# Performance work log

Hardware: AMD Instinct MI355X
Metric: run time of the kernel (lower is better)

The kernel has to match this reference:

```python
import jax, jax.numpy as jnp
import numpy as np

SIGMA = 0.002  # TreeEnergyLoss default; edge weight = exp(-||df||^2 / sigma)


def bilinear_resize(x, oh, ow):
    """F.interpolate(mode='bilinear', align_corners=False), no antialias. x: [B,C,H,W]."""
    B, C, H, W = x.shape
    if (H, W) == (oh, ow):
        return x
    def coords(o, n):
        s = (jnp.arange(o, dtype=jnp.float32) + 0.5) * (n / o) - 0.5
        s = jnp.clip(s, 0.0, n - 1.0)
        lo = jnp.floor(s).astype(jnp.int32)
        hi = jnp.minimum(lo + 1, n - 1)
        return lo, hi, s - lo.astype(jnp.float32)
    r0, r1, rf = coords(oh, H)
    c0, c1, cf = coords(ow, W)
    xr = x[:, :, r0, :] * (1.0 - rf)[None, None, :, None] + x[:, :, r1, :] * rf[None, None, :, None]
    return xr[:, :, :, c0] * (1.0 - cf) + xr[:, :, :, c1] * cf


def nearest_resize(x, oh, ow):
    B, C, H, W = x.shape
    if (H, W) == (oh, ow):
        return x
    ri = jnp.floor(jnp.arange(oh) * (H / oh)).astype(jnp.int32)
    ci = jnp.floor(jnp.arange(ow) * (W / ow)).astype(jnp.int32)
    return x[:, :, ri, :][:, :, :, ci]


def _mst_bfs_np(embed, H, W):
    """Kruskal MST on the 4-connected pixel grid (edge cost = squared L2 feature
    distance, as in MinimumSpanningTree(TreeFilter2D.norm2_distance)), then BFS
    order from vertex 0. embed: np [C,H,W]. Returns (sorted_index, sorted_parent)
    where sorted_parent is the BFS position of each vertex's parent."""
    V = H * W
    idx = np.arange(V).reshape(H, W)
    eu = np.concatenate([idx[:-1, :].ravel(), idx[:, :-1].ravel()])
    ev = np.concatenate([idx[1:, :].ravel(), idx[:, 1:].ravel()])
    f = embed.reshape(embed.shape[0], V)
    cost = ((f[:, eu] - f[:, ev]) ** 2).sum(0)
    parent = np.arange(V)
    def find(x):
        root = x
        while parent[root] != root:
            root = parent[root]
        while parent[x] != root:
            parent[x], x = root, parent[x]
        return root
    nbr = [[] for _ in range(V)]
    cnt = 0
    for e in np.argsort(cost, kind='stable'):
        u, v = int(eu[e]), int(ev[e])
        ru, rv = find(u), find(v)
        if ru != rv:
            parent[ru] = rv
            nbr[u].append(v)
            nbr[v].append(u)
            cnt += 1
            if cnt == V - 1:
                break
    sorted_index = np.empty(V, np.int32)
    sorted_parent = np.empty(V, np.int32)
    visited = np.zeros(V, bool)
    sorted_index[0] = 0; sorted_parent[0] = 0; visited[0] = True
    head, tail = 0, 1
    while head < tail:
        u = int(sorted_index[head])
        for v in nbr[u]:
            if not visited[v]:
                visited[v] = True
                sorted_index[tail] = v
                sorted_parent[tail] = head
                tail += 1
        head += 1
    return sorted_index, sorted_parent


def build_trees(embed):
    """embed: [B,C,H,W]. Host-side MST+BFS per batch element (torch.no_grad in original)."""
    e = np.asarray(jax.lax.stop_gradient(embed), dtype=np.float64)
    B, C, H, W = e.shape
    si, sp = zip(*[_mst_bfs_np(e[b], H, W) for b in range(B)])
    return jnp.asarray(np.stack(si)), jnp.asarray(np.stack(sp))


def _tree_filter_single(f, embed, sorted_index, sorted_parent):
    """Normalized tree filter: out_i = sum_j W_ij f_j / sum_j W_ij with
    W_ij = prod of exp(-||de||^2/sigma) along the unique tree path i->j.
    Computed exactly via bottom-up aggregation + top-down propagation in BFS order.
    f: [C,V], embed: [Ce,V]."""
    C, V = f.shape
    fs = f[:, sorted_index]                        # [C,V] features in BFS order
    es = embed[:, sorted_index]
    d = ((es - es[:, sorted_parent]) ** 2).sum(0)  # [V]; d[0]=0 (root self edge)
    w = jnp.exp(-d / SIGMA)                        # edge weight to parent
    # bottom-up: children have larger BFS index, so reverse order is valid.
    # extra ones-row carries the normalizer Z through the same recursion.
    S0 = jnp.concatenate([fs, jnp.ones((1, V), fs.dtype)], axis=0)
    def up(S, j):
        return S.at[:, sorted_parent[j]].add(w[j] * S[:, j]), None
    S, _ = jax.lax.scan(up, S0, jnp.arange(V - 1, 0, -1))
    # top-down: A_root = S_root; A_j = S_j + w_j * (A_parent - w_j * S_j)
    def down(A, j):
        p = sorted_parent[j]
        return A.at[:, j].set(S[:, j] + w[j] * (A[:, p] - w[j] * S[:, j])), None
    A0 = jnp.zeros_like(S).at[:, 0].set(S[:, 0])
    A, _ = jax.lax.scan(down, A0, jnp.arange(1, V))
    out_sorted = A[:C] / A[C]
    return jnp.zeros_like(f).at[:, sorted_index].set(out_sorted)


def tree_filter(feature, embed, si, sp):
    B, C, h, w = feature.shape
    out = jax.vmap(_tree_filter_single)(
        feature.reshape(B, C, h * w),
        embed.reshape(B, embed.shape[1], h * w), si, sp)
    return out.reshape(B, C, h, w)


def setup_inputs():
    key = jax.random.key(0)
    k1, k2, k3, k4 = jax.random.split(key, 4)
    preds = jax.random.normal(k1, (8, 21, 80, 80), jnp.float32)
    # scaled so exp(-||df||^2 / 0.002) gives non-degenerate edge weights
    low_feats = jax.random.uniform(k2, (8, 3, 80, 80), jnp.float32) * 0.02
    high_feats = jax.random.normal(k3, (8, 256, 80, 80), jnp.float32) * 0.002
    unlabeled_ROIs = jax.random.randint(k4, (8, 80, 80), 0, 2, dtype=jnp.int32)
    return {"preds": preds, "low_feats": low_feats,
            "high_feats": high_feats, "unlabeled_ROIs": unlabeled_ROIs}


def reference(preds, low_feats, high_feats, unlabeled_ROIs):
    B, C, h, w = preds.shape
    low = bilinear_resize(low_feats, h, w)  # under torch.no_grad in original
    roi = nearest_resize(unlabeled_ROIs[:, None].astype(jnp.float32), h, w)
    si_l, sp_l = build_trees(low)
    si_h, sp_h = build_trees(high_feats)
    prob = jax.nn.softmax(preds, axis=1)
    AS = tree_filter(prob, jax.lax.stop_gradient(low), si_l, sp_l)  # low-level tree
    AS = tree_filter(AS, high_feats, si_h, sp_h)                    # high-level tree
    N = roi.sum()
    loss = (roi * jnp.abs(prob - AS)).sum()
    return jnp.where(N > 0, loss / N, jnp.zeros((), preds.dtype))  # weight = 1.0
```

## Files before the change

### kernel.cpp

```cpp
#include <hip/hip_runtime.h>

#define BB 8
#define CP 21
#define CF 22
#define CLOW 3
#define CHIGH 256
#define WW 80
#define VV 6400
#define EVERT 6320
#define EE 12640
#define TT 16
#define SIGMA_F 0.002f
#define ROOT 3240

#define NE (VV - 1)
#define NA (2 * NE)
#define NILA 0xFFFFu
#define NB 200

__device__ __forceinline__ void edge_uv(int e, int& u, int& v) {
  if (e < EVERT) { u = e; v = e + WW; }
  else { int e2 = e - EVERT; int r = e2 / (WW - 1); int c = e2 - r * (WW - 1); u = r * WW + c; v = u + 1; }
}

__global__ void k_edgekey(const float* __restrict__ low, const float* __restrict__ high,
                          unsigned long long* __restrict__ ekey) {
  int i = blockIdx.x * blockDim.x + threadIdx.x;
  if (i >= TT * EE) return;
  int t = i / EE, e = i - t * EE;
  int u, v; edge_uv(e, u, v);
  double acc = 0.0;
  if (t < BB) {
    const float* emb = low + (size_t)t * CLOW * VV;
    for (int c = 0; c < CLOW; c++) { double d = (double)emb[c * VV + u] - (double)emb[c * VV + v]; acc += d * d; }
  } else {
    const float* emb = high + (size_t)(t - BB) * CHIGH * VV;
    for (int c = 0; c < CHIGH; c++) { double d = (double)emb[c * VV + u] - (double)emb[c * VV + v]; acc += d * d; }
  }
  unsigned long long bits = (unsigned long long)__double_as_longlong(acc);
  ekey[i] = (bits & ~0x3FFFULL) | (unsigned long long)e;
}

__global__ __launch_bounds__(1024) void k_msttree(const unsigned long long* __restrict__ ekey,
    int* __restrict__ mstU, int* __restrict__ mstV,
    int* __restrict__ ordG, int* __restrict__ spG,
    int* __restrict__ lpG, int* __restrict__ nlevG, float* __restrict__ wvp,
    const float* __restrict__ preds, float* __restrict__ prob) {
  if (blockIdx.x >= TT) {
    int i = (blockIdx.x - TT) * 1024 + threadIdx.x;
    if (i < BB * VV) {
      int b = i / VV, v = i - b * VV;
      const float* p = preds + (size_t)b * CP * VV + v;
      float m = -1e30f;
      #pragma unroll
      for (int c = 0; c < CP; c++) m = fmaxf(m, p[c * VV]);
      float e[CP], s = 0.f;
      #pragma unroll
      for (int c = 0; c < CP; c++) { float x = expf(p[c * VV] - m); e[c] = x; s += x; }
      float inv = 1.f / s;
      float* o = prob + (size_t)b * CP * VV + v;
      #pragma unroll
      for (int c = 0; c < CP; c++) o[c * VV] = e[c] * inv;
    }
    return;
  }
  int t = blockIdx.x;
  const unsigned long long* key = ekey + (size_t)t * EE;
  int* mu = mstU + t * VV;
  int* mv = mstV + t * VV;
  int tid = threadIdx.x;
  const int nt = 1024;
  int lane = tid & 63, wid = tid >> 6;

  __shared__ alignas(16) char arena[152960];
  __shared__ int lasts, spackU, spackW, scenter, smaxd, changed, cnt, necnt, nrcnt;

  int* comp = (int*)(arena + 0);
  unsigned long long* bst = (unsigned long long*)(arena + 25600);
  unsigned short* el0 = (unsigned short*)(arena + 76800);
  unsigned short* el1 = (unsigned short*)(arena + 102080);
  unsigned short* rl0 = (unsigned short*)(arena + 127360);
  unsigned short* rl1 = (unsigned short*)(arena + 140160);

  char* buf = arena;
  int* deg = (int*)(buf + 0);
  int* off = (int*)(buf + 25600);
  unsigned short* adjA = (unsigned short*)(buf + 51208);
  unsigned short* succ = (unsigned short*)(buf + 102408);
  int* pk0 = (int*)(buf + 0);
  int* pk1 = (int*)(buf + 51208);
  unsigned short* r_a = (unsigned short*)(buf + 102408);
  short* H = (short*)(buf + 51208);
  unsigned short* depthR = (unsigned short*)(buf + 76808);
  unsigned short* firstK = (unsigned short*)(buf + 89608);
  short* prefmin = (short*)(buf + 0);
  short* sufmin  = (short*)(buf + 25600);
  unsigned short* distU = (unsigned short*)(buf + 76808);
  unsigned short* parentS = (unsigned short*)(buf + 76808);
  int* lev = (int*)(buf + 0);
  int* cur = (int*)(buf + 25604);
  unsigned short* ordS = (unsigned short*)(buf + 51208);
  unsigned short* posS = (unsigned short*)(buf + 64008);
  int* part = (int*)(buf + 128016);
  short* tbl = (short*)(buf + 128272);
  unsigned short* dbuf2 = (unsigned short*)(buf + 131472);

  auto blockScanEx = [&](int s) -> int {
    int x = s;
    #pragma unroll
    for (int d = 1; d < 64; d <<= 1) { int o = __shfl_up(x, d); if (lane >= d) x += o; }
    if (lane == 63) part[wid] = x;
    __syncthreads();
    if (wid == 0) {
      int y = (lane < 16) ? part[lane] : 0;
      #pragma unroll
      for (int d = 1; d < 16; d <<= 1) { int o = __shfl_up(y, d); if (lane >= d) y += o; }
      if (lane < 16) part[lane] = y;
    }
    __syncthreads();
    int base = (wid > 0) ? part[wid - 1] : 0;
    return base + (x - s);
  };

  for (int v = tid; v < VV; v += nt) { comp[v] = v; bst[v] = ~0ULL; }
  for (int e = tid; e < EE; e += nt) el0[e] = (unsigned short)e;
  for (int v = tid; v < VV; v += nt) rl0[v] = (unsigned short)v;
  if (tid == 0) cnt = 0;
  __syncthreads();
  {
    unsigned short *els = el0, *eld = el1;
    unsigned short *rls = rl0, *rld = rl1;
    int ecnt = EE, rcnt = VV;
    for (int round = 0; round < 48 && ecnt > 0; round++) {
      if (tid == 0) { changed = 0; necnt = 0; nrcnt = 0; }
      for (int j = tid; j < ecnt; j += nt) {
        int e = els[j];
        int u, v; edge_uv(e, u, v);
        int ru = comp[u], rv = comp[v];
        if (ru != rv) { unsigned long long k = key[e]; atomicMin(&bst[ru], k); atomicMin(&bst[rv], k); }
      }
      __syncthreads();
      unsigned short* tgtJ = eld;
      for (int j = tid; j < rcnt; j += nt) {
        int c = rls[j];
        unsigned short tg = (unsigned short)NILA;
        unsigned long long k = bst[c];
        if (k != ~0ULL) {
          int e = (int)(k & 0x3FFFULL);
          int u, v; edge_uv(e, u, v);
          int cu = comp[u], cv = comp[v];
          tg = (unsigned short)((cu == c) ? cv : cu);
        }
        tgtJ[j] = tg;
      }
      __syncthreads();
      for (int j = tid; j < rcnt; j += nt) {
        int c = rls[j];
        int o = tgtJ[j];
        if (o == (int)NILA) continue;
        unsigned long long k = bst[c];
        if (bst[o] == k && c < o) continue;
        comp[c] = o;
        int slot = atomicAdd(&cnt, 1);
        int e = (int)(k & 0x3FFFULL);
        int u, v; edge_uv(e, u, v);
        mu[slot] = u; mv[slot] = v;
        changed = 1;
      }
      __syncthreads();
      if (!changed) break;
      for (int v = tid; v < VV; v += nt) {
        int c = comp[v];
        int c2 = comp[c];
        if (c2 != c) {
          int r0 = c2;
          while (true) { int n = comp[r0]; if (n == r0) break; r0 = n; }
          comp[v] = r0;
        }
      }
      __syncthreads();
      for (int j = tid; j < rcnt; j += nt) {
        int c = rls[j];
        if (comp[c] == c) { int s = atomicAdd(&nrcnt, 1); rld[s] = (unsigned short)c; bst[c] = ~0ULL; }
      }
      for (int j = tid; j < ecnt; j += nt) {
        int e = els[j];
        int u, v; edge_uv(e, u, v);
        if (comp[u] != comp[v]) { int s = atomicAdd(&necnt, 1); eld[s] = (unsigned short)e; }
      }
      __syncthreads();
      ecnt = necnt; rcnt = nrcnt;
      __syncthreads();
      unsigned short* tp = els; els = eld; eld = tp;
      tp = rls; rls = rld; rld = tp;
    }
  }
  __threadfence();
  __syncthreads();

  for (int v = tid; v < VV; v += nt) deg[v] = 0;
  __syncthreads();
  for (int e = tid; e < NE; e += nt) { atomicAdd(&deg[mu[e]], 1); atomicAdd(&deg[mv[e]], 1); }
  __syncthreads();
  {
    const int SCH = 7;
    int base = tid * SCH;
    int s = 0;
    #pragma unroll
    for (int k = 0; k < SCH; k++) { int v = base + k; if (v < VV) s += deg[v]; }
    int ex = blockScanEx(s);
    #pragma unroll
    for (int k = 0; k < SCH; k++) { int v = base + k; if (v < VV) { off[v] = ex; ex += deg[v]; } }
    if (tid == 1023) off[VV] = ex;
  }
  __syncthreads();
  for (int v = tid; v < VV; v += nt) deg[v] = off[v];
  __syncthreads();
  for (int e = tid; e < NE; e += nt) {
    int u = mu[e], v = mv[e];
    adjA[atomicAdd(&deg[u], 1)] = (unsigned short)(2 * e);
    adjA[atomicAdd(&deg[v], 1)] = (unsigned short)(2 * e + 1);
  }
  __syncthreads();
  for (int v = tid; v < VV; v += nt) {
    int b0 = off[v], dv = off[v + 1] - b0;
    for (int k = 0; k < dv; k++) {
      unsigned short a = adjA[b0 + k];
      unsigned short b = adjA[b0 + ((k + 1 == dv) ? 0 : k + 1)];
      succ[a ^ 1] = b;
    }
  }
  if (tid == 0) lasts = adjA[off[ROOT] + (off[ROOT + 1] - off[ROOT]) - 1] ^ 1;
  __syncthreads();
  if (tid == 0) succ[lasts] = (unsigned short)NILA;
  __syncthreads();
  for (int a = tid; a < NA; a += nt) {
    unsigned int n = succ[a];
    pk0[a] = ((n == NILA ? 0 : 1) << 16) | (int)n;
  }
  __syncthreads();
  {
    int* px = pk0;
    int* py = pk1;
    for (int rd = 0; rd < 14; rd++) {
      for (int a = tid; a < NA; a += nt) {
        int cur_ = px[a];
        int n = cur_ & 0xFFFF;
        if (n != (int)NILA) {
          int o = px[n];
          cur_ = (((cur_ >> 16) + (o >> 16)) << 16) | (o & 0xFFFF);
        }
        py[a] = cur_;
      }
      __syncthreads();
      int* tp = px; px = py; py = tp;
    }
    for (int a = tid; a < NA; a += nt) r_a[a] = (unsigned short)(pk0[a] >> 16);
  }
  __syncthreads();
  for (int a = tid; a < NA; a += nt) {
    int pa = NA - 1 - (int)r_a[a];
    int pb = NA - 1 - (int)r_a[a ^ 1];
    H[pa] = (pa < pb) ? (short)1 : (short)-1;
  }
  __syncthreads();
  {
    const int SCH = 13;
    int base = tid * SCH;
    int lim = base + SCH; if (lim > NA) lim = NA;
    int s = 0;
    for (int j = base; j < lim; j++) s += H[j];
    int run = blockScanEx(s);
    for (int j = base; j < lim; j++) { run += H[j]; H[j] = (short)run; }
  }
  __syncthreads();
  if (tid == 0) { spackU = 0; smaxd = 0; scenter = 0x7FFFFFFF; }
  __syncthreads();
  for (int a = tid; a < NA; a += nt) {
    int pa = NA - 1 - (int)r_a[a];
    int pb = NA - 1 - (int)r_a[a ^ 1];
    if (pa < pb) {
      int e = a >> 1;
      int head = (a & 1) ? mu[e] : mv[e];
      depthR[head] = (unsigned short)H[pa];
      firstK[head] = (unsigned short)(pa + 1);
    }
  }
  if (tid == 0) { depthR[ROOT] = 0; firstK[ROOT] = 0; }
  __syncthreads();
  {
    int loc = 0;
    for (int v = tid; v < VV; v += nt) { int p = ((int)depthR[v] << 13) | v; if (p > loc) loc = p; }
    #pragma unroll
    for (int d = 32; d > 0; d >>= 1) { int o = __shfl_down(loc, d); if (o > loc) loc = o; }
    if (lane == 0) atomicMax(&spackU, loc);
  }
  __syncthreads();
  {
    for (int seg = wid; seg < NB; seg += 16) {
      int p = seg * 64 + lane;
      int h = (p < NA) ? (int)H[p] : 32767;
      int hp = h;
      #pragma unroll
      for (int d = 1; d < 64; d <<= 1) { int o = __shfl_up(hp, d); if (lane >= d && o < hp) hp = o; }
      prefmin[p] = (short)hp;
      int hs = h;
      #pragma unroll
      for (int d = 1; d < 64; d <<= 1) { int o = __shfl_down(hs, d); if (lane + d < 64 && o < hs) hs = o; }
      sufmin[p] = (short)hs;
      if (lane == 0) tbl[seg] = (short)hs;
    }
  }
  __syncthreads();
  for (int k = 1; k < 8; k++) {
    short vv_ = 0;
    if (tid < NB) {
      int o = tid + (1 << (k - 1));
      short a = tbl[(k - 1) * NB + tid];
      short b2 = (o < NB) ? tbl[(k - 1) * NB + o] : (short)32767;
      vv_ = (a < b2) ? a : b2;
    }
    __syncthreads();
    if (tid < NB) tbl[k * NB + tid] = vv_;
    __syncthreads();
  }
  auto distq = [&](int K1, int K2) -> int {
    if (K1 == K2) return 0;
    int l = (K1 < K2 ? K1 : K2) - 1;
    int r = (K1 > K2 ? K1 : K2) - 1;
    int m = 32767;
    int l0 = l < 0 ? 0 : l;
    int bl = l0 >> 6, br = r >> 6;
    if (bl == br) {
      for (int p = l0; p <= r; p++) { int h = H[p]; if (h < m) m = h; }
    } else {
      int a = sufmin[l0], b2 = prefmin[r];
      m = a < b2 ? a : b2;
      int lo = bl + 1, hi = br - 1;
      if (lo <= hi) {
        int L = hi - lo + 1;
        int k = 31 - __builtin_clz(L);
        int c1 = tbl[k * NB + lo];
        int c2 = tbl[k * NB + hi - (1 << k) + 1];
        if (c1 < m) m = c1;
        if (c2 < m) m = c2;
      }
    }
    if (l < 0 && 0 < m) m = 0;
    int h1 = (K1 == 0) ? 0 : (int)H[K1 - 1];
    int h2 = (K2 == 0) ? 0 : (int)H[K2 - 1];
    return h1 + h2 - 2 * m;
  };
  int u = spackU & 0x1FFF;
  int Ku = firstK[u];
  if (tid == 0) spackW = 0;
  __syncthreads();
  {
    int loc = 0;
    for (int v = tid; v < VV; v += nt) {
      int d = distq(Ku, firstK[v]);
      distU[v] = (unsigned short)d;
      int p = (d << 13) | v;
      if (p > loc) loc = p;
    }
    #pragma unroll
    for (int d = 32; d > 0; d >>= 1) { int o = __shfl_down(loc, d); if (o > loc) loc = o; }
    if (lane == 0) atomicMax(&spackW, loc);
  }
  __syncthreads();
  int D = spackW >> 13;
  int w = spackW & 0x1FFF;
  int Kw = firstK[w];
  for (int v = tid; v < VV; v += nt) dbuf2[v] = (unsigned short)distq(Kw, firstK[v]);
  __syncthreads();
  {
    int half = D >> 1;
    for (int v = tid; v < VV; v += nt) {
      if ((int)distU[v] == half && (int)distU[v] + (int)dbuf2[v] == D) atomicMin(&scenter, v);
    }
  }
  __syncthreads();
  int cvert = (scenter == 0x7FFFFFFF) ? ROOT : scenter;
  int Kc = firstK[cvert];
  __syncthreads();
  {
    int loc = 0;
    for (int v = tid; v < VV; v += nt) {
      int d = distq(Kc, firstK[v]);
      dbuf2[v] = (unsigned short)d;
      if (d > loc) loc = d;
    }
    #pragma unroll
    for (int d = 32; d > 0; d >>= 1) { int o = __shfl_down(loc, d); if (o > loc) loc = o; }
    if (lane == 0) atomicMax(&smaxd, loc);
  }
  __syncthreads();
  int maxd = smaxd;
  int sTil = Kc;
  for (int a = tid; a < NA; a += nt) {
    int pa = NA - 1 - (int)r_a[a];
    int pb = NA - 1 - (int)r_a[a ^ 1];
    int pa2 = pa - sTil; if (pa2 < 0) pa2 += NA;
    int pb2 = pb - sTil; if (pb2 < 0) pb2 += NA;
    if (pa2 < pb2) {
      int e = a >> 1;
      int head = (a & 1) ? mu[e] : mv[e];
      int tail = (a & 1) ? mv[e] : mu[e];
      parentS[head] = (unsigned short)tail;
    }
  }
  if (tid == 0) parentS[cvert] = (unsigned short)cvert;
  __syncthreads();
  for (int d = tid; d <= VV; d += nt) lev[d] = 0;
  __syncthreads();
  for (int v = tid; v < VV; v += nt) atomicAdd(&lev[dbuf2[v]], 1);
  __syncthreads();
  {
    const int SCH = 7;
    int base = tid * SCH;
    int s = 0;
    #pragma unroll
    for (int k = 0; k < SCH; k++) { int d = base + k; if (d <= VV) s += lev[d]; }
    int ex = blockScanEx(s);
    #pragma unroll
    for (int k = 0; k < SCH; k++) {
      int d = base + k;
      if (d <= VV) {
        int st = ex;
        ex += lev[d];
        if (d < VV) cur[d] = st;
        lpG[t * (VV + 1) + d] = st;
      }
    }
  }
  __syncthreads();
  for (int v = tid; v < VV; v += nt) {
    int d = dbuf2[v];
    int slot = atomicAdd(&cur[d], 1);
    ordS[slot] = (unsigned short)v;
    posS[v] = (unsigned short)slot;
  }
  __syncthreads();
  for (int j = tid; j < VV; j += nt) {
    int v = ordS[j];
    int pv = parentS[v];
    ordG[t * VV + j] = v;
    spG[t * VV + j] = posS[pv];
    float wout;
    if (v == pv) {
      wout = 1.0f;
    } else {
      int a = v < pv ? v : pv;
      int diff = v < pv ? pv - v : v - pv;
      int e;
      if (diff == WW) e = a;
      else { int r = a / WW, c = a - r * WW; e = EVERT + r * (WW - 1) + c; }
      unsigned long long k = key[e];
      double cost = __longlong_as_double((long long)(k & ~0x3FFFULL));
      wout = expf(-(float)cost / SIGMA_F);
    }
    wvp[t * VV + j] = wout;
  }
  if (tid == 0) nlevG[t] = maxd + 1;
}

__global__ __launch_bounds__(1024) void k_filter_pc(const float* __restrict__ Fsrc, float* __restrict__ Araw,
    const float* __restrict__ wvp, const int* __restrict__ ordG, const int* __restrict__ spG,
    const int* __restrict__ lpG, const int* __restrict__ nlevG, int treeBase) {
  int blk = blockIdx.x;
  int b = blk / CF, ch = blk - b * CF;
  int t = treeBase + b;
  __shared__ alignas(16) char arena[140816];
  float2* ab0 = (float2*)(arena);
  float2* ab1 = (float2*)(arena + 51200);
  float*  S   = (float*)(arena + 51200);
  float*  w   = (float*)(arena + 76800);
  unsigned short* sp0 = (unsigned short*)(arena + 102400);
  unsigned short* sp1 = (unsigned short*)(arena + 115200);
  unsigned short* lpS = (unsigned short*)(arena + 128000);
  const int* ord = ordG + t * VV;
  const int* spt = spG + t * VV;
  const float* wsrc = wvp + t * VV;
  const int* lp = lpG + t * (VV + 1);
  int tid = threadIdx.x;
  const int nt = 1024;
  int NL = nlevG[t];
  for (int j = tid; j <= NL; j += nt) lpS[j] = (unsigned short)lp[j];
  const bool norm_in = (treeBase != 0);
  for (int j = tid; j < VV; j += nt) {
    sp0[j] = (unsigned short)spt[j];
    w[j] = wsrc[j];
    float val;
    if (ch < CP) {
      int v = ord[j];
      if (!norm_in) val = Fsrc[((size_t)b * CP + ch) * VV + v];
      else          val = Fsrc[((size_t)b * CF + ch) * VV + v] / Fsrc[((size_t)b * CF + CP) * VV + v];
    } else val = 1.0f;
    S[j] = val;
  }
  __syncthreads();
  if (tid < 64) {
    int s1 = lpS[NL];
    int s0 = lpS[NL - 1];
    for (int l = NL - 1; l >= 1; l--) {
      int s0n = (l > 1) ? (int)lpS[l - 1] : 0;
      for (int j = s0 + tid; j < s1; j += 64) {
        atomicAdd(&S[sp0[j]], w[j] * S[j]);
      }
      asm volatile("s_waitcnt lgkmcnt(0)" ::: "memory");
      __builtin_amdgcn_sched_barrier(0);
      s1 = s0; s0 = s0n;
    }
  }
  __syncthreads();
  for (int j = tid; j < VV; j += nt) {
    float wv = w[j];
    float a = (j == 0) ? 0.f : wv;
    float bv = (j == 0) ? S[0] : S[j] * (1.f - wv * wv);
    ab0[j] = make_float2(a, bv);
  }
  __syncthreads();
  int rounds = 0;
  { int d = 1; while (d < NL) { d <<= 1; rounds++; } }
  float2 *abs_ = ab0, *abd_ = ab1;
  unsigned short *ps_ = sp0, *pd_ = sp1;
  for (int r = 0; r < rounds; r++) {
    for (int j = tid; j < VV; j += nt) {
      float2 m = abs_[j];
      int p = ps_[j];
      float2 o = m;
      int pn = p;
      if (m.x != 0.f) {
        float2 mp = abs_[p];
        pn = ps_[p];
        o.x = m.x * mp.x;
        o.y = fmaf(m.x, mp.y, m.y);
      }
      abd_[j] = o;
      pd_[j] = (unsigned short)pn;
    }
    __syncthreads();
    float2* tf = abs_; abs_ = abd_; abd_ = tf;
    unsigned short* tu = ps_; ps_ = pd_; pd_ = tu;
  }
  float* Ob = Araw + ((size_t)b * CF + ch) * VV;
  for (int j = tid; j < VV; j += nt) Ob[ord[j]] = abs_[j].y;
}

__global__ void k_loss(const float* __restrict__ prob, const float* __restrict__ Araw2,
                       const int* __restrict__ roi, double* __restrict__ acc,
                       unsigned int* __restrict__ done, float* __restrict__ out) {
  int i = blockIdx.x * blockDim.x + threadIdx.x;
  int tid = threadIdx.x;
  double s = 0.0, n = 0.0;
  if (i < BB * VV) {
    int b = i / VV, v = i - b * VV;
    if (roi[i] != 0) {
      n = 1.0;
      const float* pb = prob + (size_t)b * CP * VV + v;
      const float* ab = Araw2 + (size_t)b * CF * VV + v;
      float inv = 1.0f / ab[CP * VV];
      float ls = 0.f;
      #pragma unroll
      for (int c = 0; c < CP; c++) ls += fabsf(pb[c * VV] - ab[c * VV] * inv);
      s = (double)ls;
    }
  }
  __shared__ double rs[256], rn[256];
  __shared__ bool amLast;
  rs[tid] = s; rn[tid] = n;
  __syncthreads();
  for (int d = 128; d > 0; d >>= 1) {
    if (tid < d) { rs[tid] += rs[tid + d]; rn[tid] += rn[tid + d]; }
    __syncthreads();
  }
  if (tid == 0) {
    atomicAdd(&acc[0], rs[0]);
    atomicAdd(&acc[1], rn[0]);
    __threadfence();
    unsigned int prev = atomicAdd(done, 1u);
    amLast = (prev == gridDim.x - 1);
  }
  __syncthreads();
  if (amLast && tid == 0) {
    __threadfence();
    double ss = acc[0], nn = acc[1];
    out[0] = (nn > 0.0) ? (float)(ss / nn) : 0.0f;
  }
}

extern "C" void kernel_launch(void* const* d_in, const int* in_sizes, int n_in,
                              void* d_out, int out_size, void* d_ws, size_t ws_size,
                              hipStream_t stream) {
  const float* preds = (const float*)d_in[0];
  const float* low   = (const float*)d_in[1];
  const float* high  = (const float*)d_in[2];
  const int*   roi   = (const int*)d_in[3];
  float* out = (float*)d_out;

  char* w = (char*)d_ws;
  size_t off = 0;
  auto alloc = [&](size_t bytes) -> void* {
    void* p = w + off;
    off += (bytes + 255) & ~(size_t)255;
    return p;
  };
  float* prob  = (float*)alloc((size_t)BB * CP * VV * 4);
  float* Araw1 = (float*)alloc((size_t)BB * CF * VV * 4);
  float* Araw2 = (float*)alloc((size_t)BB * CF * VV * 4);
  unsigned long long* ekey = (unsigned long long*)alloc((size_t)TT * EE * 8);
  int* mstU = (int*)alloc((size_t)TT * VV * 4);
  int* mstV = (int*)alloc((size_t)TT * VV * 4);
  int* ordG = (int*)alloc((size_t)TT * VV * 4);
  int* spG  = (int*)alloc((size_t)TT * VV * 4);
  int* lpG  = (int*)alloc((size_t)TT * (VV + 1) * 4);
  int* nlev = (int*)alloc((size_t)TT * 4);
  float* wvp = (float*)alloc((size_t)TT * VV * 4);
  double* acc = (double*)alloc(32);

  hipMemsetAsync(acc, 0, 32, stream);

  const int nSoft = (BB * VV + 1023) / 1024;
  k_edgekey<<<(TT * EE + 255) / 256, 256, 0, stream>>>(low, high, ekey);
  k_msttree<<<TT + nSoft, 1024, 0, stream>>>(ekey, mstU, mstV, ordG, spG, lpG, nlev, wvp, preds, prob);
  k_filter_pc<<<BB * CF, 1024, 0, stream>>>(prob,  Araw1, wvp, ordG, spG, lpG, nlev, 0);
  k_filter_pc<<<BB * CF, 1024, 0, stream>>>(Araw1, Araw2, wvp, ordG, spG, lpG, nlev, BB);
  k_loss<<<(BB * VV + 255) / 256, 256, 0, stream>>>(prob, Araw2, roi, acc,
      (unsigned int*)(acc + 2), out);
}
```

Before: 268.9 us.

## Use sublist-based list ranking for Euler tour instead of full pointer jumping

Replaces 14 rounds of pointer jumping over all ~12.8k Euler-tour arcs with a sparse ruling-set approach. Every 8th arc, plus the head arc, starts a sublist. Each sublist is walked serially to record local offsets and sublist ids, then only the ~1600 sublist heads are ranked with 11 rounds of pointer jumping. Ranks are then expanded back per arc. This cuts shared-memory traffic and barriers per round, at the cost of serial walks of variable length (about 8 on average) and some thread imbalance.

```diff
diff --git a/kernel.cpp b/kernel.cpp
--- a/kernel.cpp
+++ b/kernel.cpp
@@ -73,7 +73,7 @@
   int lane = tid & 63, wid = tid >> 6;
 
   __shared__ alignas(16) char arena[152960];
-  __shared__ int lasts, spackU, spackW, scenter, smaxd, changed, cnt, necnt, nrcnt;
+  __shared__ int lasts, headS, spackU, spackW, scenter, smaxd, changed, cnt, necnt, nrcnt;
 
   int* comp = (int*)(arena + 0);
   unsigned long long* bst = (unsigned long long*)(arena + 25600);
@@ -87,8 +87,10 @@
   int* off = (int*)(buf + 25600);
   unsigned short* adjA = (unsigned short*)(buf + 51208);
   unsigned short* succ = (unsigned short*)(buf + 102408);
-  int* pk0 = (int*)(buf + 0);
-  int* pk1 = (int*)(buf + 51208);
+  unsigned short* subId = (unsigned short*)(buf + 0);
+  unsigned short* locOf = (unsigned short*)(buf + 25600);
+  int* pkS0 = (int*)(buf + 51208);
+  int* pkS1 = (int*)(buf + 57864);
   unsigned short* r_a = (unsigned short*)(buf + 102408);
   short* H = (short*)(buf + 51208);
   unsigned short* depthR = (unsigned short*)(buf + 76808);
@@ -230,32 +232,54 @@
       succ[a ^ 1] = b;
     }
   }
-  if (tid == 0) lasts = adjA[off[ROOT] + (off[ROOT + 1] - off[ROOT]) - 1] ^ 1;
+  if (tid == 0) {
+    lasts = adjA[off[ROOT] + (off[ROOT + 1] - off[ROOT]) - 1] ^ 1;
+    headS = adjA[off[ROOT]];
+  }
   __syncthreads();
   if (tid == 0) succ[lasts] = (unsigned short)NILA;
   __syncthreads();
-  for (int a = tid; a < NA; a += nt) {
-    unsigned int n = succ[a];
-    pk0[a] = ((n == NILA ? 0 : 1) << 16) | (int)n;
-  }
-  __syncthreads();
-  {
-    int* px = pk0;
-    int* py = pk1;
-    for (int rd = 0; rd < 14; rd++) {
-      for (int a = tid; a < NA; a += nt) {
-        int cur_ = px[a];
-        int n = cur_ & 0xFFFF;
-        if (n != (int)NILA) {
+  int headA = headS;
+  int headExtra = (headA & 7) ? 1 : 0;
+  int NS = 1600 + headExtra;
+  for (int k = tid; k < NS; k += nt) {
+    int a = (k < 1600) ? (k << 3) : headA;
+    int off_ = 0;
+    for (int step = 0; step < NA; step++) {
+      subId[a] = (unsigned short)k;
+      locOf[a] = (unsigned short)off_;
+      off_++;
+      int n = succ[a];
+      if (n == (int)NILA) { pkS0[k] = (off_ << 16) | 0xFFFF; break; }
+      if ((n & 7) == 0)   { pkS0[k] = (off_ << 16) | (n >> 3); break; }
+      a = n;
+    }
+  }
+  __syncthreads();
+  int* pxF;
+  {
+    int* px = pkS0;
+    int* py = pkS1;
+    for (int rd = 0; rd < 11; rd++) {
+      for (int k2 = tid; k2 < NS; k2 += nt) {
+        int c = px[k2];
+        int n = c & 0xFFFF;
+        if (n != 0xFFFF) {
           int o = px[n];
-          cur_ = (((cur_ >> 16) + (o >> 16)) << 16) | (o & 0xFFFF);
+          c = (((c >> 16) + (o >> 16)) << 16) | (o & 0xFFFF);
         }
-        py[a] = cur_;
+        py[k2] = c;
       }
       __syncthreads();
       int* tp = px; px = py; py = tp;
     }
-    for (int a = tid; a < NA; a += nt) r_a[a] = (unsigned short)(pk0[a] >> 16);
+    pxF = px;
+  }
+  for (int a = tid; a < NA; a += nt) {
+    int k = subId[a];
+    int totFrom = pxF[k] >> 16;
+    int pos = (NA - totFrom) + (int)locOf[a];
+    r_a[a] = (unsigned short)(NA - 1 - pos);
   }
   __syncthreads();
   for (int a = tid; a < NA; a += nt) {
```

Measured after the change: 266.2 us. About the same (-1.0%).
